# Performance work log

Hardware: AMD Instinct MI355X
Metric: run time of the kernel (lower is better)

The kernel has to match this reference:

```python
import jax, jax.numpy as jnp
import numpy as np

B, H, W = 128, 32, 32
INF = 1e9
EPS = 1e-6  # strictly positive weights -> dist strictly decreases along backtrack (no tie cycles)
OFFS = np.array([(-1, -1), (-1, 0), (-1, 1), (0, -1), (0, 1), (1, -1), (1, 0), (1, 1)], dtype=np.int32)


def _neighbor_min(d):
    # d: [B,H,W] -> per-cell min over 8-neighborhood (INF outside the grid)
    p = jnp.pad(d, ((0, 0), (1, 1), (1, 1)), constant_values=INF)
    sh = jnp.stack([p[:, 1 + dr:1 + dr + H, 1 + dc:1 + dc + W] for dr, dc in OFFS], axis=0)
    return jnp.min(sh, axis=0)


def solve(weights, source, target):
    """Dijkstra/A*(h=0)-equivalent shortest path on an 8-connected grid.
    Entering cell v costs weights[v]; returns a [B,H,W] 0/1 mask of the optimal path
    (source and target cells included). Computed exactly via Bellman-Ford relaxation
    (H*W sweeps >= max hop count) followed by greedy min-dist backtracking.
    """
    w = weights + EPS
    b = jnp.arange(B)
    sr, sc = source[:, 0], source[:, 1]
    ws = w[b, sr, sc]
    dist0 = jnp.full((B, H, W), INF, w.dtype).at[b, sr, sc].set(ws)

    def bf_step(dist, _):
        return jnp.minimum(dist, w + _neighbor_min(dist)), None

    dist, _ = jax.lax.scan(bf_step, dist0, None, length=H * W)

    dist_flat = dist.reshape(B, H * W)
    offs = jnp.asarray(OFFS)  # [8,2]
    hw = jnp.array([H, W], offs.dtype)

    def bt_step(carry, _):
        pos, mask, done = carry            # pos [B,2], mask [B,H,W], done [B]
        r, c = pos[:, 0], pos[:, 1]
        mask = mask.at[b, r, c].max((~done).astype(mask.dtype))
        done = done | ((r == sr) & (c == sc))
        cand = pos[:, None, :] + offs[None]               # [B,8,2]
        valid = ((cand >= 0) & (cand < hw)).all(-1)       # [B,8]
        cr = jnp.clip(cand[..., 0], 0, H - 1)
        cc = jnp.clip(cand[..., 1], 0, W - 1)
        dvals = jnp.take_along_axis(dist_flat, cr * W + cc, axis=1)
        dvals = jnp.where(valid, dvals, INF)
        j = jnp.argmin(dvals, axis=1)                     # predecessor = min-dist neighbor
        nxt = jnp.stack([cr[b, j], cc[b, j]], axis=1)
        pos = jnp.where(done[:, None], pos, nxt)
        return (pos, mask, done), None

    mask0 = jnp.zeros((B, H, W), weights.dtype)
    done0 = jnp.zeros((B,), bool)
    (_, paths, _), _ = jax.lax.scan(bt_step, (target.astype(offs.dtype), mask0, done0), None, length=H * W)
    return paths


def setup_inputs() -> dict:
    key = jax.random.key(0)
    k1, k2, k3 = jax.random.split(key, 3)
    return {
        "weights": jax.random.uniform(k1, (B, H, W), jnp.float32),
        "source": jax.random.randint(k2, (B, 2), 0, H),
        "target": jax.random.randint(k3, (B, 2), 0, H),
    }


def reference(weights, source, target):
    # BBAStar.forward: paths come straight from a_star_batch (the autograd.Function
    # forward is identity on paths); exp_nodes is solver-internal bookkeeping and is
    # not part of the math being differentiated, so we return the path masks.
    return solve(weights, source, target)
```

## Files before the change

kernel.cpp:

```cpp
#include <hip/hip_runtime.h>

#define GH 32
#define GW 32
#define P  34
#define NP (P * P)
#define INFV 1000000000.0f
#define EPSV 1e-6f


#define NMIN8(ul,uu,ur,ll,rr,dl,dd,dr) \
    fminf(fminf(fminf(fminf((ul),(uu)),(ur)), fminf(fminf((ll),(rr)),(dl))), fminf((dd),(dr)))

#define RELAXF(i,j) {                                                         \
    const float ul = ((i)==0) ? top[(j)]   : (((j)==0) ? lft[(i)-1] : t[(i)-1][(j)-1]); \
    const float uu = ((i)==0) ? top[(j)+1] : t[(i)-1][(j)];                    \
    const float ur = ((i)==0) ? top[(j)+2] : (((j)==3) ? rgt[(i)-1] : t[(i)-1][(j)+1]); \
    const float ll = ((j)==0) ? lft[(i)]   : t[(i)][(j)-1];                    \
    const float rr = ((j)==3) ? rgt[(i)]   : t[(i)][(j)+1];                    \
    const float dl = ((i)==3) ? bot[(j)]   : (((j)==0) ? lft[(i)+1] : t[(i)+1][(j)-1]); \
    const float dd = ((i)==3) ? bot[(j)+1] : t[(i)+1][(j)];                    \
    const float dr = ((i)==3) ? bot[(j)+2] : (((j)==3) ? rgt[(i)+1] : t[(i)+1][(j)+1]); \
    const float nd = w[i][j] + NMIN8(ul,uu,ur,ll,rr,dl,dd,dr);                \
    t[i][j] = fminf(t[i][j], nd);                                             \
}

#define RELAXB(i,j) {                                                         \
    const float ul = ((i)==0) ? top[(j)]   : (((j)==0) ? lft[(i)-1] : t[(i)-1][(j)-1]); \
    const float uu = ((i)==0) ? top[(j)+1] : t[(i)-1][(j)];                    \
    const float ur = ((i)==0) ? top[(j)+2] : (((j)==3) ? rgt[(i)-1] : t[(i)-1][(j)+1]); \
    const float ll = ((j)==0) ? lft[(i)]   : t[(i)][(j)-1];                    \
    const float rr = ((j)==3) ? rgt[(i)]   : t[(i)][(j)+1];                    \
    const float dl = ((i)==3) ? bot[(j)]   : (((j)==0) ? lft[(i)+1] : t[(i)+1][(j)-1]); \
    const float dd = ((i)==3) ? bot[(j)+1] : t[(i)+1][(j)];                    \
    const float dr = ((i)==3) ? bot[(j)+2] : (((j)==3) ? rgt[(i)+1] : t[(i)+1][(j)+1]); \
    const float nd = w[i][j] + NMIN8(ul,uu,ur,ll,rr,dl,dd,dr);                \
    ch = ch || (nd < t[i][j]);                                                \
    t[i][j] = fminf(t[i][j], nd);                                             \
}

#define RINGREAD {                                                            \
    _Pragma("unroll")                                                         \
    for (int k = 0; k < 6; ++k) {                                             \
        top[k] = d[base - P - 1 + k];                                         \
        bot[k] = d[base + 4 * P - 1 + k];                                     \
    }                                                                         \
    _Pragma("unroll")                                                         \
    for (int i = 0; i < 4; ++i) {                                             \
        lft[i] = d[base + i * P - 1];                                         \
        rgt[i] = d[base + i * P + 4];                                         \
    }                                                                         \
}

#define BORDERWRITE {                                                         \
    _Pragma("unroll")                                                         \
    for (int j = 0; j < 4; ++j) {                                             \
        d[base + j]         = t[0][j];                                        \
        d[base + 3 * P + j] = t[3][j];                                        \
    }                                                                         \
    d[base + P]         = t[1][0];                                            \
    d[base + 2 * P]     = t[2][0];                                            \
    d[base + P + 3]     = t[1][3];                                            \
    d[base + 2 * P + 3] = t[2][3];                                            \
}

__global__ __launch_bounds__(64)
void bbastar_kernel(const float* __restrict__ weights,
                    const int* __restrict__ source,
                    const int* __restrict__ target,
                    float* __restrict__ out) {
    __shared__ float d[NP];

    const int b   = blockIdx.x;
    const int tid = threadIdx.x;
    const int tr  = tid >> 3;
    const int tc  = tid & 7;
    const int r0  = tr << 2;
    const int c0  = tc << 2;
    const int base = (r0 + 1) * P + (c0 + 1);

    const int sr  = source[2 * b];
    const int sc  = source[2 * b + 1];

    float w[4][4], t[4][4];
    const float* wb = weights + b * (GH * GW);
    #pragma unroll
    for (int i = 0; i < 4; ++i) {
        const float4 v = *(const float4*)(wb + (r0 + i) * GW + c0);
        w[i][0] = v.x + EPSV; w[i][1] = v.y + EPSV;
        w[i][2] = v.z + EPSV; w[i][3] = v.w + EPSV;
    }

    float4* ob4 = (float4*)(out + b * (GH * GW));
    #pragma unroll
    for (int k = 0; k < 4; ++k) ob4[tid + 64 * k] = make_float4(0.f, 0.f, 0.f, 0.f);

    for (int i = tid; i < NP; i += 64) d[i] = INFV;
    #pragma unroll
    for (int i = 0; i < 4; ++i)
        #pragma unroll
        for (int j = 0; j < 4; ++j) t[i][j] = INFV;
    __syncthreads();

    #pragma unroll
    for (int i = 0; i < 4; ++i)
        #pragma unroll
        for (int j = 0; j < 4; ++j)
            if (sr == r0 + i && sc == c0 + j) {
                t[i][j] = w[i][j];
                d[base + i * P + j] = w[i][j];
            }
    __syncthreads();

    float top[6], bot[6], lft[4], rgt[4];
    for (int pair = 0; pair < 2048; ++pair) {
        RINGREAD
        #pragma unroll
        for (int i = 0; i < 4; ++i)
            #pragma unroll
            for (int j = 0; j < 4; ++j) RELAXF(i, j)
        BORDERWRITE
        __syncthreads();

        RINGREAD
        bool ch = false;
        #pragma unroll
        for (int i = 3; i >= 0; --i)
            #pragma unroll
            for (int j = 3; j >= 0; --j) RELAXB(i, j)
        BORDERWRITE
        __syncthreads();
        if (__ballot(ch) == 0ULL) break;
    }

    #pragma unroll
    for (int i = 0; i < 4; ++i)
        #pragma unroll
        for (int j = 0; j < 4; ++j)
            d[base + i * P + j] = t[i][j];
    __syncthreads();

    if (tid == 0) {
        const int drr[8] = {-1, -1, -1,  0, 0,  1, 1, 1};
        const int dcc[8] = {-1,  0,  1, -1, 1, -1, 0, 1};
        int pr = target[2 * b];
        int pc = target[2 * b + 1];
        float* ob = out + b * (GH * GW);
        for (int step = 0; step < GH * GW; ++step) {
            ob[pr * GW + pc] = 1.0f;
            if (pr == sr && pc == sc) break;
            float best = INFV;
            int bj = 0;
            #pragma unroll
            for (int j = 0; j < 8; ++j) {
                const float vv = d[(pr + drr[j] + 1) * P + (pc + dcc[j] + 1)];
                if (vv < best) { best = vv; bj = j; }
            }
            pr += drr[bj];
            pc += dcc[bj];
        }
    }
}

extern "C" void kernel_launch(void* const* d_in, const int* in_sizes, int n_in,
                              void* d_out, int out_size, void* d_ws, size_t ws_size,
                              hipStream_t stream) {
    const float* weights = (const float*)d_in[0];
    const int*   source  = (const int*)d_in[1];
    const int*   target  = (const int*)d_in[2];
    float*       out     = (float*)d_out;
    const int B = in_sizes[0] / (GH * GW);
    bbastar_kernel<<<B, 64, 0, stream>>>(weights, source, target, out);
}
```

Before: 76.35 us.

## Stop relaxation once target distance is settled and precompute backtrack directions

The convergence test no longer requires the whole grid to stop changing. It tracks the smallest distance that changed in each window and stops once every change lies above the target's current distance. Because weights are positive, such changes cannot affect cells on the optimal path. The check runs once per four sweeps instead of every two, which cuts ballot and branch overhead but may run up to two extra sweeps. All threads now compute each cell's predecessor direction in parallel into shared bytes, so the single-thread backtrack does one byte lookup per step instead of eight shared-memory reads.

```diff
diff --git a/kernel.cpp b/kernel.cpp
--- a/kernel.cpp
+++ b/kernel.cpp
@@ -8,10 +8,7 @@
 #define EPSV 1e-6f
 
 
-#define NMIN8(ul,uu,ur,ll,rr,dl,dd,dr) \
-    fminf(fminf(fminf(fminf((ul),(uu)),(ur)), fminf(fminf((ll),(rr)),(dl))), fminf((dd),(dr)))
-
-#define RELAXF(i,j) {                                                         \
+#define NBRS(i,j) \
     const float ul = ((i)==0) ? top[(j)]   : (((j)==0) ? lft[(i)-1] : t[(i)-1][(j)-1]); \
     const float uu = ((i)==0) ? top[(j)+1] : t[(i)-1][(j)];                    \
     const float ur = ((i)==0) ? top[(j)+2] : (((j)==3) ? rgt[(i)-1] : t[(i)-1][(j)+1]); \
@@ -19,26 +16,18 @@
     const float rr = ((j)==3) ? rgt[(i)]   : t[(i)][(j)+1];                    \
     const float dl = ((i)==3) ? bot[(j)]   : (((j)==0) ? lft[(i)+1] : t[(i)+1][(j)-1]); \
     const float dd = ((i)==3) ? bot[(j)+1] : t[(i)+1][(j)];                    \
-    const float dr = ((i)==3) ? bot[(j)+2] : (((j)==3) ? rgt[(i)+1] : t[(i)+1][(j)+1]); \
-    const float nd = w[i][j] + NMIN8(ul,uu,ur,ll,rr,dl,dd,dr);                \
-    t[i][j] = fminf(t[i][j], nd);                                             \
-}
+    const float dr = ((i)==3) ? bot[(j)+2] : (((j)==3) ? rgt[(i)+1] : t[(i)+1][(j)+1]);
 
-#define RELAXB(i,j) {                                                         \
-    const float ul = ((i)==0) ? top[(j)]   : (((j)==0) ? lft[(i)-1] : t[(i)-1][(j)-1]); \
-    const float uu = ((i)==0) ? top[(j)+1] : t[(i)-1][(j)];                    \
-    const float ur = ((i)==0) ? top[(j)+2] : (((j)==3) ? rgt[(i)-1] : t[(i)-1][(j)+1]); \
-    const float ll = ((j)==0) ? lft[(i)]   : t[(i)][(j)-1];                    \
-    const float rr = ((j)==3) ? rgt[(i)]   : t[(i)][(j)+1];                    \
-    const float dl = ((i)==3) ? bot[(j)]   : (((j)==0) ? lft[(i)+1] : t[(i)+1][(j)-1]); \
-    const float dd = ((i)==3) ? bot[(j)+1] : t[(i)+1][(j)];                    \
-    const float dr = ((i)==3) ? bot[(j)+2] : (((j)==3) ? rgt[(i)+1] : t[(i)+1][(j)+1]); \
-    const float nd = w[i][j] + NMIN8(ul,uu,ur,ll,rr,dl,dd,dr);                \
-    ch = ch || (nd < t[i][j]);                                                \
-    t[i][j] = fminf(t[i][j], nd);                                             \
-}
+#define NMIN8 \
+    fminf(fminf(fminf(fminf(ul,uu),ur), fminf(fminf(ll,rr),dl)), fminf(dd,dr))
 
-#define RINGREAD {                                                            \
+#define RELAXT(i,j) { NBRS(i,j)                                               \
+    const float old = t[(i)][(j)];                                            \
+    const float nd  = w[(i)][(j)] + NMIN8;                                    \
+    cm = fminf(cm, (nd < old) ? nd : INFV);                                   \
+    t[(i)][(j)] = fminf(old, nd); }
+
+#define RINGREAD                                                              \
     _Pragma("unroll")                                                         \
     for (int k = 0; k < 6; ++k) {                                             \
         top[k] = d[base - P - 1 + k];                                         \
@@ -48,10 +37,11 @@
     for (int i = 0; i < 4; ++i) {                                             \
         lft[i] = d[base + i * P - 1];                                         \
         rgt[i] = d[base + i * P + 4];                                         \
-    }                                                                         \
-}
+    }
 
-#define BORDERWRITE {                                                         \
+#define WR(i,j) d[base + (i)*P + (j)] = t[(i)][(j)];
+
+#define BORDERWRITE                                                           \
     _Pragma("unroll")                                                         \
     for (int j = 0; j < 4; ++j) {                                             \
         d[base + j]         = t[0][j];                                        \
@@ -60,15 +50,41 @@
     d[base + P]         = t[1][0];                                            \
     d[base + 2 * P]     = t[2][0];                                            \
     d[base + P + 3]     = t[1][3];                                            \
-    d[base + 2 * P + 3] = t[2][3];                                            \
-}
+    d[base + 2 * P + 3] = t[2][3];
+
+#define UNITF { float top[6], bot[6], lft[4], rgt[4]; RINGREAD                \
+    _Pragma("unroll") for (int i = 0; i < 4; ++i)                             \
+    _Pragma("unroll") for (int j = 0; j < 4; ++j) RELAXT(i, j)                \
+    BORDERWRITE __syncthreads(); }
+
+#define UNITB { float top[6], bot[6], lft[4], rgt[4]; RINGREAD                \
+    _Pragma("unroll") for (int i = 3; i >= 0; --i)                            \
+    _Pragma("unroll") for (int j = 3; j >= 0; --j) RELAXT(i, j)               \
+    BORDERWRITE __syncthreads(); }
+
+#define UNITB_PUB { float top[6], bot[6], lft[4], rgt[4]; RINGREAD            \
+    _Pragma("unroll") for (int i = 3; i >= 0; --i)                            \
+    _Pragma("unroll") for (int j = 3; j >= 0; --j) RELAXT(i, j)               \
+    BORDERWRITE WR(1,1) WR(1,2) WR(2,1) WR(2,2) __syncthreads(); }
+
+#define DIRC(i,j) { NBRS(i,j)                                                 \
+    float best = ul; int bj = 0;                                              \
+    if (uu < best) { best = uu; bj = 1; }                                     \
+    if (ur < best) { best = ur; bj = 2; }                                     \
+    if (ll < best) { best = ll; bj = 3; }                                     \
+    if (rr < best) { best = rr; bj = 4; }                                     \
+    if (dl < best) { best = dl; bj = 5; }                                     \
+    if (dd < best) { best = dd; bj = 6; }                                     \
+    if (dr < best) { best = dr; bj = 7; }                                     \
+    dirs[(r0 + (i)) * GW + (c0 + (j))] = (unsigned char)bj; }
 
 __global__ __launch_bounds__(64)
 void bbastar_kernel(const float* __restrict__ weights,
                     const int* __restrict__ source,
                     const int* __restrict__ target,
                     float* __restrict__ out) {
-    __shared__ float d[NP];
+    __shared__ alignas(16) float d[NP];
+    __shared__ unsigned char dirs[GH * GW];
 
     const int b   = blockIdx.x;
     const int tid = threadIdx.x;
@@ -80,6 +96,9 @@
 
     const int sr  = source[2 * b];
     const int sc  = source[2 * b + 1];
+    const int tgr = target[2 * b];
+    const int tgc = target[2 * b + 1];
+    const int tga = (tgr + 1) * P + (tgc + 1);
 
     float w[4][4], t[4][4];
     const float* wb = weights + b * (GH * GW);
@@ -94,7 +113,12 @@
     #pragma unroll
     for (int k = 0; k < 4; ++k) ob4[tid + 64 * k] = make_float4(0.f, 0.f, 0.f, 0.f);
 
-    for (int i = tid; i < NP; i += 64) d[i] = INFV;
+    {
+        float4* d4 = (float4*)d;
+        #pragma unroll
+        for (int i = tid; i < NP / 4; i += 64)
+            d4[i] = make_float4(INFV, INFV, INFV, INFV);
+    }
     #pragma unroll
     for (int i = 0; i < 4; ++i)
         #pragma unroll
@@ -111,52 +135,43 @@
             }
     __syncthreads();
 
-    float top[6], bot[6], lft[4], rgt[4];
-    for (int pair = 0; pair < 2048; ++pair) {
-        RINGREAD
-        #pragma unroll
-        for (int i = 0; i < 4; ++i)
-            #pragma unroll
-            for (int j = 0; j < 4; ++j) RELAXF(i, j)
-        BORDERWRITE
-        __syncthreads();
-
-        RINGREAD
-        bool ch = false;
-        #pragma unroll
-        for (int i = 3; i >= 0; --i)
-            #pragma unroll
-            for (int j = 3; j >= 0; --j) RELAXB(i, j)
-        BORDERWRITE
-        __syncthreads();
-        if (__ballot(ch) == 0ULL) break;
+    float cm = INFV;
+    for (int win = 0; win < 1024; ++win) {
+        UNITF
+        UNITB
+        UNITF
+        UNITB_PUB
+        const float dt = d[tga];
+        if (__ballot(cm <= dt) == 0ULL) break;
+        cm = INFV;
     }
 
     #pragma unroll
     for (int i = 0; i < 4; ++i)
         #pragma unroll
-        for (int j = 0; j < 4; ++j)
-            d[base + i * P + j] = t[i][j];
+        for (int j = 0; j < 4; ++j) WR(i, j)
+    __syncthreads();
+
+    {
+        float top[6], bot[6], lft[4], rgt[4];
+        RINGREAD
+        #pragma unroll
+        for (int i = 0; i < 4; ++i)
+            #pragma unroll
+            for (int j = 0; j < 4; ++j) DIRC(i, j)
+    }
     __syncthreads();
 
     if (tid == 0) {
-        const int drr[8] = {-1, -1, -1,  0, 0,  1, 1, 1};
-        const int dcc[8] = {-1,  0,  1, -1, 1, -1, 0, 1};
-        int pr = target[2 * b];
-        int pc = target[2 * b + 1];
+        int pr = tgr;
+        int pc = tgc;
         float* ob = out + b * (GH * GW);
         for (int step = 0; step < GH * GW; ++step) {
             ob[pr * GW + pc] = 1.0f;
             if (pr == sr && pc == sc) break;
-            float best = INFV;
-            int bj = 0;
-            #pragma unroll
-            for (int j = 0; j < 8; ++j) {
-                const float vv = d[(pr + drr[j] + 1) * P + (pc + dcc[j] + 1)];
-                if (vv < best) { best = vv; bj = j; }
-            }
-            pr += drr[bj];
-            pc += dcc[bj];
+            const int bj = dirs[pr * GW + pc];
+            pr += ((0xE0 >> bj) & 1) - ((0x07 >> bj) & 1);
+            pc += ((0x94 >> bj) & 1) - ((0x29 >> bj) & 1);
         }
     }
 }
```

New measurement: 73.67 us. 3.5% less time.
